# Kernel tuning notes

Hardware: AMD Instinct MI355X
Metric: run time of the kernel (lower is better)

Reference implementation:

```python
import jax, jax.numpy as jnp
import numpy as np

NUM_NODES = 9
HIDDEN = 512


def _vortex_mask(num_nodes=NUM_NODES):
    mask = np.ones((num_nodes, num_nodes), dtype=np.float32)
    for src, dst in [(0, 1), (1, 3), (3, 7), (7, 6), (6, 4), (4, 0)]:
        if src < num_nodes and dst < num_nodes:
            mask[src, dst] = mask[dst, src] = 2.0
    for a, b in [(0, 7), (1, 6), (3, 4), (2, 5)]:
        if a < num_nodes and b < num_nodes:
            mask[a, b] = mask[b, a] = 2.0
    if num_nodes > 8:
        mask[8, :] = 1.5
        mask[:, 8] = 1.5
    return jnp.asarray(mask)


def setup_inputs() -> dict:
    key = jax.random.key(0)
    ks = jax.random.split(key, 10)
    B = 16384
    s = 1.0 / np.sqrt(HIDDEN)
    return {
        "node_features": jax.random.normal(ks[0], (B, NUM_NODES, HIDDEN), jnp.float32),
        "pos_enc": jax.random.normal(ks[1], (NUM_NODES, HIDDEN), jnp.float32) * 0.1,
        "Wq": jax.random.uniform(ks[2], (HIDDEN, HIDDEN), jnp.float32, -s, s),
        "bq": jax.random.uniform(ks[3], (HIDDEN,), jnp.float32, -s, s),
        "Wk": jax.random.uniform(ks[4], (HIDDEN, HIDDEN), jnp.float32, -s, s),
        "bk": jax.random.uniform(ks[5], (HIDDEN,), jnp.float32, -s, s),
        "Wv": jax.random.uniform(ks[6], (HIDDEN, HIDDEN), jnp.float32, -s, s),
        "bv": jax.random.uniform(ks[7], (HIDDEN,), jnp.float32, -s, s),
        "Wg": jax.random.uniform(ks[8], (HIDDEN, 1), jnp.float32, -s, s),
        "bg": jax.random.uniform(ks[9], (1,), jnp.float32, -s, s),
    }


def reference(node_features, pos_enc, Wq, bq, Wk, bk, Wv, bv, Wg, bg):
    mask = _vortex_mask()  # [N, N] constant buffer
    x = node_features + pos_enc[None]  # [B, N, D]
    q = x @ Wq + bq
    k = x @ Wk + bk
    v = x @ Wv + bv
    scale = 1.0 / jnp.sqrt(jnp.asarray(HIDDEN, q.dtype))
    scores = jnp.einsum("bnd,bmd->bnm", q, k) * scale * mask
    weights = jax.nn.softmax(scores, axis=-1)
    out = jnp.einsum("bnm,bmd->bnd", weights, v)
    # central-node gating (num_nodes > 8)
    central = node_features[:, 8]  # [B, D]
    gate = jax.nn.sigmoid(central @ Wg + bg)[:, None]  # [B, 1, 1]
    out = out * (1.0 - gate) + central[:, None, :] * gate
    return out
```

## Files before the change

kernel.cpp:

```cpp
#include <hip/hip_runtime.h>
#include <stdint.h>

typedef __attribute__((ext_vector_type(8))) short short8;
typedef __attribute__((ext_vector_type(4))) short short4v;
typedef __attribute__((ext_vector_type(4))) float f32x4;

#define AS1 __attribute__((address_space(1)))
#define AS3 __attribute__((address_space(3)))

#define SM_X     0
#define SM_U     81920
#define SM_WB1   (SM_U + 16384)
#define SM_BW    135168
#define SM_S     151808
#define SM_MASK  154400
#define SM_A     154728
#define SM_B     155048
#define SM_G     155368
#define SM_TOT   155400

static __device__ __forceinline__ short f2bf(float f){
  unsigned u = __builtin_bit_cast(unsigned, f);
  u += 0x7FFFu + ((u >> 16) & 1u);
  return (short)(u >> 16);
}
static __device__ __forceinline__ float wred64(float v){
  #pragma unroll
  for (int o = 1; o < 64; o <<= 1) v += __shfl_xor(v, o, 64);
  return v;
}
static __device__ __forceinline__ size_t prep_off(int k, int n){
  return ((size_t)(((k >> 5) * 2 + (n >> 8)) * 16 + ((n >> 4) & 15))) * 512
       + (size_t)((((k >> 3) & 3) * 16 + (n & 15)) * 8 + (k & 7));
}

__global__ __launch_bounds__(256) void vortex_prep(
    const float* __restrict__ Wq, const float* __restrict__ bq,
    const float* __restrict__ Wk, const float* __restrict__ bk,
    const float* __restrict__ Wv,
    short* __restrict__ Mp, short* __restrict__ Vp,
    float* __restrict__ uvec, float* __restrict__ wvec, float* __restrict__ cval)
{
  const int blk = blockIdx.x, tid = threadIdx.x;
  if (blk < 256){
    const int wv = tid >> 6, lane = tid & 63;
    const int tile = blk * 4 + wv, ti = tile >> 5, tj = tile & 31;
    const int r = lane & 15, g = lane >> 4;
    f32x4 acc = {0.f, 0.f, 0.f, 0.f};
    for (int k0 = 0; k0 < 512; k0 += 32){
      const float* ap = Wq + (ti*16 + r)*512 + k0 + g*8;
      const float* bp = Wk + (tj*16 + r)*512 + k0 + g*8;
      f32x4 a0 = *(const f32x4*)ap, a1 = *(const f32x4*)(ap+4);
      f32x4 b0 = *(const f32x4*)bp, b1 = *(const f32x4*)(bp+4);
      short8 av, bv8;
      av[0]=f2bf(a0[0]); av[1]=f2bf(a0[1]); av[2]=f2bf(a0[2]); av[3]=f2bf(a0[3]);
      av[4]=f2bf(a1[0]); av[5]=f2bf(a1[1]); av[6]=f2bf(a1[2]); av[7]=f2bf(a1[3]);
      bv8[0]=f2bf(b0[0]); bv8[1]=f2bf(b0[1]); bv8[2]=f2bf(b0[2]); bv8[3]=f2bf(b0[3]);
      bv8[4]=f2bf(b1[0]); bv8[5]=f2bf(b1[1]); bv8[6]=f2bf(b1[2]); bv8[7]=f2bf(b1[3]);
      acc = __builtin_amdgcn_mfma_f32_16x16x32_bf16(av, bv8, acc, 0, 0, 0);
    }
    #pragma unroll
    for (int rr = 0; rr < 4; ++rr){
      int d1 = ti*16 + g*4 + rr, d2 = tj*16 + r;
      Mp[prep_off(d1, d2)] = f2bf(acc[rr]);
    }
  } else if (blk < 320){
    int base = ((blk - 256) * 256 + tid) * 16;
    #pragma unroll
    for (int e = 0; e < 16; ++e){
      int idx = base + e;
      Vp[prep_off(idx >> 9, idx & 511)] = f2bf(Wv[idx]);
    }
  } else {
    for (int d = tid; d < 512; d += 256){
      float su = 0.f, sw = 0.f;
      for (int j = 0; j < 512; ++j){
        su = fmaf(Wq[d*512 + j], bk[j], su);
        sw = fmaf(Wk[d*512 + j], bq[j], sw);
      }
      uvec[d] = su; wvec[d] = sw;
    }
    if (tid == 0){
      float s = 0.f;
      for (int j = 0; j < 512; ++j) s = fmaf(bq[j], bk[j], s);
      *cval = s;
    }
  }
}

static __device__ __forceinline__ void stage2(const char* g, char* l){
  __builtin_amdgcn_global_load_lds((const AS1 unsigned*)g,        (AS3 unsigned*)l,        16, 0, 0);
  __builtin_amdgcn_global_load_lds((const AS1 unsigned*)(g+1024), (AS3 unsigned*)(l+1024), 16, 0, 0);
}

static __device__ __forceinline__ void gemm_kloop(const char* prep, int p, char* sm,
                                                  int w, int lane, f32x4 (&acc)[5][2])
{
  const int l15 = lane & 15, lg = lane >> 4;
  const int goff = w*2048 + lane*16;
  char* wb0 = sm + SM_U;
  char* wb1 = sm + SM_WB1;
  stage2(prep + (size_t)p*16384 + goff, wb0 + w*2048);
  __syncthreads();
  for (int ks = 0; ks < 16; ++ks){
    char* rb = (ks & 1) ? wb1 : wb0;
    if (ks < 15){
      char* nb = (ks & 1) ? wb0 : wb1;
      stage2(prep + (size_t)((ks+1)*2 + p)*16384 + goff, nb + w*2048);
    }
    short8 af[5], bfr[2];
    #pragma unroll
    for (int mf = 0; mf < 5; ++mf){
      const int row = mf*16 + l15;
      af[mf] = *(const short8*)(sm + (row << 10) + (((ks << 6) | (lg << 4)) ^ ((row & 7) << 4)));
    }
    bfr[0] = *(const short8*)(rb + (2*w  )*1024 + lane*16);
    bfr[1] = *(const short8*)(rb + (2*w+1)*1024 + lane*16);
    #pragma unroll
    for (int mf = 0; mf < 5; ++mf){
      acc[mf][0] = __builtin_amdgcn_mfma_f32_16x16x32_bf16(af[mf], bfr[0], acc[mf][0], 0,0,0);
      acc[mf][1] = __builtin_amdgcn_mfma_f32_16x16x32_bf16(af[mf], bfr[1], acc[mf][1], 0,0,0);
    }
    __syncthreads();
  }
}

__global__ __launch_bounds__(512, 2) void vortex_main(
    const float* __restrict__ nf, const float* __restrict__ pos,
    const float* __restrict__ bv, const float* __restrict__ Wg, const float* __restrict__ bgp,
    const short* __restrict__ Mp, const short* __restrict__ Vp,
    const float* __restrict__ uvec, const float* __restrict__ wvec, const float* __restrict__ cptr,
    float* __restrict__ out)
{
  __shared__ __align__(16) char sm[SM_TOT];
  const int tid = threadIdx.x;
  const int w = tid >> 6, lane = tid & 63;
  const int l15 = lane & 15, lg = lane >> 4;
  const int wg = blockIdx.x;

  short8 creg;
  {
    const int col0 = lane * 8;
    f32x4 u0 = *(const f32x4*)(uvec + col0), u1 = *(const f32x4*)(uvec + col0 + 4);
    f32x4 v0 = *(const f32x4*)(wvec + col0), v1 = *(const f32x4*)(wvec + col0 + 4);
    f32x4 g0 = *(const f32x4*)(Wg   + col0), g1 = *(const f32x4*)(Wg   + col0 + 4);
    const size_t gb = ((size_t)wg*8 + w) * 9 * 512;
    for (int rl = 0; rl < 9; ++rl){
      f32x4 n0 = *(const f32x4*)(nf + gb + rl*512 + col0);
      f32x4 n1 = *(const f32x4*)(nf + gb + rl*512 + col0 + 4);
      f32x4 p0 = *(const f32x4*)(pos + rl*512 + col0);
      f32x4 p1 = *(const f32x4*)(pos + rl*512 + col0 + 4);
      f32x4 x0 = n0 + p0, x1 = n1 + p1;
      short8 xb;
      xb[0]=f2bf(x0[0]); xb[1]=f2bf(x0[1]); xb[2]=f2bf(x0[2]); xb[3]=f2bf(x0[3]);
      xb[4]=f2bf(x1[0]); xb[5]=f2bf(x1[1]); xb[6]=f2bf(x1[2]); xb[7]=f2bf(x1[3]);
      const int row = w*9 + rl;
      *(short8*)(sm + (row << 10) + ((lane << 4) ^ ((row & 7) << 4))) = xb;
      float pa = x0[0]*u0[0]+x0[1]*u0[1]+x0[2]*u0[2]+x0[3]*u0[3]
               + x1[0]*u1[0]+x1[1]*u1[1]+x1[2]*u1[2]+x1[3]*u1[3];
      float pb = x0[0]*v0[0]+x0[1]*v0[1]+x0[2]*v0[2]+x0[3]*v0[3]
               + x1[0]*v1[0]+x1[1]*v1[1]+x1[2]*v1[2]+x1[3]*v1[3];
      pa = wred64(pa); pb = wred64(pb);
      if (lane == 0){
        ((float*)(sm + SM_A))[row] = pa;
        ((float*)(sm + SM_B))[row] = pb;
      }
      if (rl == 8){
        short8 cb;
        cb[0]=f2bf(n0[0]); cb[1]=f2bf(n0[1]); cb[2]=f2bf(n0[2]); cb[3]=f2bf(n0[3]);
        cb[4]=f2bf(n1[0]); cb[5]=f2bf(n1[1]); cb[6]=f2bf(n1[2]); cb[7]=f2bf(n1[3]);
        creg = cb;
        float pg = n0[0]*g0[0]+n0[1]*g0[1]+n0[2]*g0[2]+n0[3]*g0[3]
                 + n1[0]*g1[0]+n1[1]*g1[1]+n1[2]*g1[2]+n1[3]*g1[3];
        pg = wred64(pg);
        if (lane == 0){
          float z = pg + bgp[0];
          ((float*)(sm + SM_G))[w] = 1.f / (1.f + __expf(-z));
        }
      }
    }
    {
      const int row = 72 + w;
      short8 z = {0,0,0,0,0,0,0,0};
      *(short8*)(sm + (row << 10) + ((lane << 4) ^ ((row & 7) << 4))) = z;
    }
    for (int t = tid; t < 1040; t += 512){
      f32x4 z = {0.f,0.f,0.f,0.f};
      *(f32x4*)(sm + SM_BW + t*16) = z;
    }
    if (tid < 81){
      int n = tid / 9, m = tid - (tid/9)*9;
      bool edge = ((n%3)==0 && (m%3)==1) || ((n%3)==1 && (m%3)==0)
               || (n==2 && m==5) || (n==5 && m==2);
      float mv = (n==8 || m==8) ? 1.5f : (edge ? 2.0f : 1.0f);
      ((float*)(sm + SM_MASK))[tid] = mv;
    }
  }
  __syncthreads();

  const int mi0 = (w + 1) / 3,  nj0 = w - 2*mi0;
  const int mi1 = (w + 9) / 3,  nj1 = (w + 8) - 2*mi1;

  f32x4 sacc0 = {0.f,0.f,0.f,0.f}, sacc1 = {0.f,0.f,0.f,0.f};

  for (int p = 0; p < 2; ++p){
    f32x4 tacc[5][2];
    #pragma unroll
    for (int mf = 0; mf < 5; ++mf){
      tacc[mf][0] = (f32x4){0.f,0.f,0.f,0.f};
      tacc[mf][1] = (f32x4){0.f,0.f,0.f,0.f};
    }
    gemm_kloop((const char*)Mp, p, sm, w, lane, tacc);
    #pragma unroll
    for (int mf = 0; mf < 5; ++mf)
      #pragma unroll
      for (int nfi = 0; nfi < 2; ++nfi){
        const int col = w*32 + nfi*16 + l15;
        #pragma unroll
        for (int r = 0; r < 4; ++r){
          const int row = mf*16 + lg*4 + r;
          *(short*)(sm + SM_U + (row << 9) + ((col*2) ^ ((row & 7) << 4))) = f2bf(tacc[mf][nfi][r]);
        }
      }
    __syncthreads();
    #pragma unroll
    for (int ks = 0; ks < 8; ++ks){
      const int ar = mi0*16 + l15;
      short8 a = *(const short8*)(sm + (ar<<10) + (((p<<9)|(ks<<6)|(lg<<4)) ^ ((ar&7)<<4)));
      const int br = nj0*16 + l15;
      short8 b = *(const short8*)(sm + SM_U + (br<<9) + (((ks<<6)|(lg<<4)) ^ ((br&7)<<4)));
      sacc0 = __builtin_amdgcn_mfma_f32_16x16x32_bf16(a, b, sacc0, 0,0,0);
    }
    if (w < 5){
      #pragma unroll
      for (int ks = 0; ks < 8; ++ks){
        const int ar = mi1*16 + l15;
        short8 a = *(const short8*)(sm + (ar<<10) + (((p<<9)|(ks<<6)|(lg<<4)) ^ ((ar&7)<<4)));
        const int br = nj1*16 + l15;
        short8 b = *(const short8*)(sm + SM_U + (br<<9) + (((ks<<6)|(lg<<4)) ^ ((br&7)<<4)));
        sacc1 = __builtin_amdgcn_mfma_f32_16x16x32_bf16(a, b, sacc1, 0,0,0);
      }
    }
    __syncthreads();
  }

  {
    #pragma unroll
    for (int r = 0; r < 4; ++r){
      const int m = mi0*16 + lg*4 + r, n = nj0*16 + l15;
      if (m < 72 && n < 72){
        const int bm = (m*57)>>9, bn = (n*57)>>9;
        if (bm == bn)
          ((float*)(sm + SM_S))[bm*81 + (n - bn*9)*9 + (m - bm*9)] = sacc0[r];
      }
    }
    if (w < 5){
      #pragma unroll
      for (int r = 0; r < 4; ++r){
        const int m = mi1*16 + lg*4 + r, n = nj1*16 + l15;
        if (m < 72 && n < 72){
          const int bm = (m*57)>>9, bn = (n*57)>>9;
          if (bm == bn)
            ((float*)(sm + SM_S))[bm*81 + (n - bn*9)*9 + (m - bm*9)] = sacc1[r];
        }
      }
    }
  }
  __syncthreads();

  if (tid < 72){
    const int b = tid / 9, np = tid - b*9;
    const float g  = ((float*)(sm + SM_G))[b];
    const float an = ((float*)(sm + SM_A))[b*9 + np];
    const float cv = cptr[0];
    const float scl = 0.04419417382415922f;
    float vals[9]; float mx = -1e30f;
    #pragma unroll
    for (int m = 0; m < 9; ++m){
      float s = (((float*)(sm + SM_S))[b*81 + np*9 + m] + an
                 + ((float*)(sm + SM_B))[b*9 + m] + cv)
              * scl * ((float*)(sm + SM_MASK))[np*9 + m];
      vals[m] = s; mx = fmaxf(mx, s);
    }
    float sum = 0.f;
    #pragma unroll
    for (int m = 0; m < 9; ++m){ vals[m] = __expf(vals[m] - mx); sum += vals[m]; }
    const float wsc = (1.f - g) / sum;
    const int rowg = b*9 + np;
    #pragma unroll
    for (int m = 0; m < 9; ++m)
      *(short*)(sm + SM_BW + rowg*208 + (b*9 + m)*2) = f2bf(vals[m]*wsc);
    *(short*)(sm + SM_BW + rowg*208 + (80 + b)*2) = f2bf(g);
  }
  __syncthreads();

  for (int p = 0; p < 2; ++p){
    f32x4 vacc[5][2];
    #pragma unroll
    for (int mf = 0; mf < 5; ++mf){
      vacc[mf][0] = (f32x4){0.f,0.f,0.f,0.f};
      vacc[mf][1] = (f32x4){0.f,0.f,0.f,0.f};
    }
    gemm_kloop((const char*)Vp, p, sm, w, lane, vacc);
    #pragma unroll
    for (int mf = 0; mf < 5; ++mf)
      #pragma unroll
      for (int nfi = 0; nfi < 2; ++nfi){
        const int d  = w*32 + nfi*16 + l15;
        const int m0 = mf*16 + lg*4;
        short4v pk;
        pk[0]=f2bf(vacc[mf][nfi][0]); pk[1]=f2bf(vacc[mf][nfi][1]);
        pk[2]=f2bf(vacc[mf][nfi][2]); pk[3]=f2bf(vacc[mf][nfi][3]);
        *(short4v*)(sm + SM_U + d*208 + m0*2) = pk;
      }
    #pragma unroll
    for (int j = 0; j < 8; ++j){
      const int d = lane*8 + j;
      if ((d >> 8) == p)
        *(short*)(sm + SM_U + (d & 255)*208 + (80 + w)*2) = creg[j];
    }
    __syncthreads();
    f32x4 oacc[5][2];
    #pragma unroll
    for (int mf = 0; mf < 5; ++mf){
      oacc[mf][0] = (f32x4){0.f,0.f,0.f,0.f};
      oacc[mf][1] = (f32x4){0.f,0.f,0.f,0.f};
    }
    #pragma unroll
    for (int ks = 0; ks < 3; ++ks){
      short8 aw[5], bw0, bw1;
      #pragma unroll
      for (int mf = 0; mf < 5; ++mf){
        const int n = mf*16 + l15;
        aw[mf] = *(const short8*)(sm + SM_BW + n*208 + ks*64 + lg*16);
      }
      bw0 = *(const short8*)(sm + SM_U + (w*32      + l15)*208 + ks*64 + lg*16);
      bw1 = *(const short8*)(sm + SM_U + (w*32 + 16 + l15)*208 + ks*64 + lg*16);
      #pragma unroll
      for (int mf = 0; mf < 5; ++mf){
        oacc[mf][0] = __builtin_amdgcn_mfma_f32_16x16x32_bf16(aw[mf], bw0, oacc[mf][0], 0,0,0);
        oacc[mf][1] = __builtin_amdgcn_mfma_f32_16x16x32_bf16(aw[mf], bw1, oacc[mf][1], 0,0,0);
      }
    }
    #pragma unroll
    for (int nfi = 0; nfi < 2; ++nfi){
      const int d = p*256 + w*32 + nfi*16 + l15;
      const float bvd = bv[d];
      #pragma unroll
      for (int mf = 0; mf < 5; ++mf)
        #pragma unroll
        for (int r = 0; r < 4; ++r){
          const int n = mf*16 + lg*4 + r;
          if (n < 72){
            const int b = (n*57)>>9;
            const float g = ((float*)(sm + SM_G))[b];
            out[((size_t)wg*72 + n)*512 + d] = oacc[mf][nfi][r] + (1.f - g)*bvd;
          }
        }
    }
    __syncthreads();
  }
}

extern "C" void kernel_launch(void* const* d_in, const int* in_sizes, int n_in,
                              void* d_out, int out_size, void* d_ws, size_t ws_size,
                              hipStream_t stream)
{
  const float* nf  = (const float*)d_in[0];
  const float* pos = (const float*)d_in[1];
  const float* Wq  = (const float*)d_in[2];
  const float* bq  = (const float*)d_in[3];
  const float* Wk  = (const float*)d_in[4];
  const float* bk  = (const float*)d_in[5];
  const float* Wv  = (const float*)d_in[6];
  const float* bv  = (const float*)d_in[7];
  const float* Wg  = (const float*)d_in[8];
  const float* bg  = (const float*)d_in[9];
  float* out = (float*)d_out;
  char* ws = (char*)d_ws;
  short* Mp   = (short*)(ws);
  short* Vp   = (short*)(ws + 524288);
  float* uvec = (float*)(ws + 1048576);
  float* wvec = (float*)(ws + 1050624);
  float* cval = (float*)(ws + 1052672);
  if (ws_size < 1052676) return;

  const int B = in_sizes[0] / (9 * 512);
  vortex_prep<<<321, 256, 0, stream>>>(Wq, bq, Wk, bk, Wv, Mp, Vp, uvec, wvec, cval);
  vortex_main<<<B/8, 512, 0, stream>>>(nf, pos, bv, Wg, bg, Mp, Vp, uvec, wvec, cval, out);
}
```

Before: 899.4 us.

## Load GEMM B fragments directly to registers and parallelize bias-vector prep

```diff
diff --git a/kernel.cpp b/kernel.cpp
--- a/kernel.cpp
+++ b/kernel.cpp
@@ -5,12 +5,8 @@
 typedef __attribute__((ext_vector_type(4))) short short4v;
 typedef __attribute__((ext_vector_type(4))) float f32x4;
 
-#define AS1 __attribute__((address_space(1)))
-#define AS3 __attribute__((address_space(3)))
-
 #define SM_X     0
 #define SM_U     81920
-#define SM_WB1   (SM_U + 16384)
 #define SM_BW    135168
 #define SM_S     151808
 #define SM_MASK  154400
@@ -28,6 +24,10 @@
   #pragma unroll
   for (int o = 1; o < 64; o <<= 1) v += __shfl_xor(v, o, 64);
   return v;
+}
+static __device__ __forceinline__ float dot8(f32x4 a0, f32x4 a1, f32x4 b0, f32x4 b1){
+  return a0[0]*b0[0]+a0[1]*b0[1]+a0[2]*b0[2]+a0[3]*b0[3]
+       + a1[0]*b1[0]+a1[1]*b1[1]+a1[2]*b1[2]+a1[3]*b1[3];
 }
 static __device__ __forceinline__ size_t prep_off(int k, int n){
   return ((size_t)(((k >> 5) * 2 + (n >> 8)) * 16 + ((n >> 4) & 15))) * 512
@@ -42,8 +42,8 @@
     float* __restrict__ uvec, float* __restrict__ wvec, float* __restrict__ cval)
 {
   const int blk = blockIdx.x, tid = threadIdx.x;
+  const int wv = tid >> 6, lane = tid & 63;
   if (blk < 256){
-    const int wv = tid >> 6, lane = tid & 63;
     const int tile = blk * 4 + wv, ti = tile >> 5, tj = tile & 31;
     const int r = lane & 15, g = lane >> 4;
     f32x4 acc = {0.f, 0.f, 0.f, 0.f};
@@ -71,57 +71,48 @@
       int idx = base + e;
       Vp[prep_off(idx >> 9, idx & 511)] = f2bf(Wv[idx]);
     }
+  } else if (blk < 448){
+    const int d = (blk - 320) * 4 + wv;
+    const float* wqr = Wq + (size_t)d*512 + lane*8;
+    const float* wkr = Wk + (size_t)d*512 + lane*8;
+    f32x4 q0 = *(const f32x4*)wqr,          q1 = *(const f32x4*)(wqr + 4);
+    f32x4 k0 = *(const f32x4*)wkr,          k1 = *(const f32x4*)(wkr + 4);
+    f32x4 bk0 = *(const f32x4*)(bk + lane*8), bk1 = *(const f32x4*)(bk + lane*8 + 4);
+    f32x4 bq0 = *(const f32x4*)(bq + lane*8), bq1 = *(const f32x4*)(bq + lane*8 + 4);
+    float su = wred64(dot8(q0, q1, bk0, bk1));
+    float sw = wred64(dot8(k0, k1, bq0, bq1));
+    if (lane == 0){ uvec[d] = su; wvec[d] = sw; }
   } else {
-    for (int d = tid; d < 512; d += 256){
-      float su = 0.f, sw = 0.f;
-      for (int j = 0; j < 512; ++j){
-        su = fmaf(Wq[d*512 + j], bk[j], su);
-        sw = fmaf(Wk[d*512 + j], bq[j], sw);
-      }
-      uvec[d] = su; wvec[d] = sw;
-    }
-    if (tid == 0){
-      float s = 0.f;
-      for (int j = 0; j < 512; ++j) s = fmaf(bq[j], bk[j], s);
-      *cval = s;
-    }
-  }
-}
-
-static __device__ __forceinline__ void stage2(const char* g, char* l){
-  __builtin_amdgcn_global_load_lds((const AS1 unsigned*)g,        (AS3 unsigned*)l,        16, 0, 0);
-  __builtin_amdgcn_global_load_lds((const AS1 unsigned*)(g+1024), (AS3 unsigned*)(l+1024), 16, 0, 0);
-}
-
-static __device__ __forceinline__ void gemm_kloop(const char* prep, int p, char* sm,
-                                                  int w, int lane, f32x4 (&acc)[5][2])
+    if (wv == 0){
+      f32x4 a0 = *(const f32x4*)(bq + lane*8), a1 = *(const f32x4*)(bq + lane*8 + 4);
+      f32x4 b0 = *(const f32x4*)(bk + lane*8), b1 = *(const f32x4*)(bk + lane*8 + 4);
+      float s = wred64(dot8(a0, a1, b0, b1));
+      if (lane == 0) *cval = s;
+    }
+  }
+}
+
+static __device__ __forceinline__ void gemm_kloop_reg(const char* __restrict__ prep, int p,
+                                                      const char* sm, int w, int lane,
+                                                      f32x4 (&acc)[5][2])
 {
   const int l15 = lane & 15, lg = lane >> 4;
-  const int goff = w*2048 + lane*16;
-  char* wb0 = sm + SM_U;
-  char* wb1 = sm + SM_WB1;
-  stage2(prep + (size_t)p*16384 + goff, wb0 + w*2048);
-  __syncthreads();
+  #pragma unroll
   for (int ks = 0; ks < 16; ++ks){
-    char* rb = (ks & 1) ? wb1 : wb0;
-    if (ks < 15){
-      char* nb = (ks & 1) ? wb0 : wb1;
-      stage2(prep + (size_t)((ks+1)*2 + p)*16384 + goff, nb + w*2048);
-    }
-    short8 af[5], bfr[2];
+    const char* bbase = prep + (size_t)((ks*2 + p)*16 + 2*w) * 1024 + lane*16;
+    short8 b0 = *(const short8*)(bbase);
+    short8 b1 = *(const short8*)(bbase + 1024);
+    short8 af[5];
     #pragma unroll
     for (int mf = 0; mf < 5; ++mf){
       const int row = mf*16 + l15;
       af[mf] = *(const short8*)(sm + (row << 10) + (((ks << 6) | (lg << 4)) ^ ((row & 7) << 4)));
     }
-    bfr[0] = *(const short8*)(rb + (2*w  )*1024 + lane*16);
-    bfr[1] = *(const short8*)(rb + (2*w+1)*1024 + lane*16);
-    #pragma unroll
-    for (int mf = 0; mf < 5; ++mf){
-      acc[mf][0] = __builtin_amdgcn_mfma_f32_16x16x32_bf16(af[mf], bfr[0], acc[mf][0], 0,0,0);
-      acc[mf][1] = __builtin_amdgcn_mfma_f32_16x16x32_bf16(af[mf], bfr[1], acc[mf][1], 0,0,0);
-    }
-    __syncthreads();
+    #pragma unroll
+    for (int mf = 0; mf < 5; ++mf){
+      acc[mf][0] = __builtin_amdgcn_mfma_f32_16x16x32_bf16(af[mf], b0, acc[mf][0], 0,0,0);
+      acc[mf][1] = __builtin_amdgcn_mfma_f32_16x16x32_bf16(af[mf], b1, acc[mf][1], 0,0,0);
+    }
   }
 }
 
@@ -156,11 +147,8 @@
       xb[4]=f2bf(x1[0]); xb[5]=f2bf(x1[1]); xb[6]=f2bf(x1[2]); xb[7]=f2bf(x1[3]);
       const int row = w*9 + rl;
       *(short8*)(sm + (row << 10) + ((lane << 4) ^ ((row & 7) << 4))) = xb;
-      float pa = x0[0]*u0[0]+x0[1]*u0[1]+x0[2]*u0[2]+x0[3]*u0[3]
-               + x1[0]*u1[0]+x1[1]*u1[1]+x1[2]*u1[2]+x1[3]*u1[3];
-      float pb = x0[0]*v0[0]+x0[1]*v0[1]+x0[2]*v0[2]+x0[3]*v0[3]
-               + x1[0]*v1[0]+x1[1]*v1[1]+x1[2]*v1[2]+x1[3]*v1[3];
-      pa = wred64(pa); pb = wred64(pb);
+      float pa = wred64(dot8(x0, x1, u0, u1));
+      float pb = wred64(dot8(x0, x1, v0, v1));
       if (lane == 0){
         ((float*)(sm + SM_A))[row] = pa;
         ((float*)(sm + SM_B))[row] = pb;
@@ -170,9 +158,7 @@
         cb[0]=f2bf(n0[0]); cb[1]=f2bf(n0[1]); cb[2]=f2bf(n0[2]); cb[3]=f2bf(n0[3]);
         cb[4]=f2bf(n1[0]); cb[5]=f2bf(n1[1]); cb[6]=f2bf(n1[2]); cb[7]=f2bf(n1[3]);
         creg = cb;
-        float pg = n0[0]*g0[0]+n0[1]*g0[1]+n0[2]*g0[2]+n0[3]*g0[3]
-                 + n1[0]*g1[0]+n1[1]*g1[1]+n1[2]*g1[2]+n1[3]*g1[3];
-        pg = wred64(pg);
+        float pg = wred64(dot8(n0, n1, g0, g1));
         if (lane == 0){
           float z = pg + bgp[0];
           ((float*)(sm + SM_G))[w] = 1.f / (1.f + __expf(-z));
@@ -210,7 +196,7 @@
       tacc[mf][0] = (f32x4){0.f,0.f,0.f,0.f};
       tacc[mf][1] = (f32x4){0.f,0.f,0.f,0.f};
     }
-    gemm_kloop((const char*)Mp, p, sm, w, lane, tacc);
+    gemm_kloop_reg((const char*)Mp, p, sm, w, lane, tacc);
     #pragma unroll
     for (int mf = 0; mf < 5; ++mf)
       #pragma unroll
@@ -301,7 +287,7 @@
       vacc[mf][0] = (f32x4){0.f,0.f,0.f,0.f};
       vacc[mf][1] = (f32x4){0.f,0.f,0.f,0.f};
     }
-    gemm_kloop((const char*)Vp, p, sm, w, lane, vacc);
+    gemm_kloop_reg((const char*)Vp, p, sm, w, lane, vacc);
     #pragma unroll
     for (int mf = 0; mf < 5; ++mf)
       #pragma unroll
@@ -318,6 +304,10 @@
       const int d = lane*8 + j;
       if ((d >> 8) == p)
         *(short*)(sm + SM_U + (d & 255)*208 + (80 + w)*2) = creg[j];
+    }
+    if (tid < 256){
+      f32x4 z = {0.f,0.f,0.f,0.f};
+      *(f32x4*)(sm + SM_U + tid*208 + 176) = z;
     }
     __syncthreads();
     f32x4 oacc[5][2];
@@ -386,6 +376,6 @@
   if (ws_size < 1052676) return;
 
   const int B = in_sizes[0] / (9 * 512);
-  vortex_prep<<<321, 256, 0, stream>>>(Wq, bq, Wk, bk, Wv, Mp, Vp, uvec, wvec, cval);
+  vortex_prep<<<449, 256, 0, stream>>>(Wq, bq, Wk, bk, Wv, Mp, Vp, uvec, wvec, cval);
   vortex_main<<<B/8, 512, 0, stream>>>(nf, pos, bv, Wg, bg, Mp, Vp, uvec, wvec, cval, out);
 }
```

Result: faster. 778.6 us (-13.4%).
